# Kernel optimization log

Measured on AMD Instinct MI355X. Metric: run time of the kernel, lower is better.

## Reference

```python
import jax, jax.numpy as jnp
import numpy as np

N_USERS = 50000
N_ITEMS = 50000
N_NODES = N_USERS + N_ITEMS
NNZ = 1600000
EMB = 64
N_LAYERS = 3
REG = 1e-5
BATCH = 4096


def setup_inputs() -> dict:
    key = jax.random.key(0)
    ks = jax.random.split(key, 12)
    s = 1.0 / np.sqrt(EMB)
    return {
        "user_emb": jax.random.normal(ks[0], (N_USERS, EMB), jnp.float32) * s,
        "item_emb": jax.random.normal(ks[1], (N_ITEMS, EMB), jnp.float32) * s,
        "W_gc": jax.random.normal(ks[2], (N_LAYERS, EMB, EMB), jnp.float32) * s,
        "b_gc": jax.random.normal(ks[3], (N_LAYERS, 1, EMB), jnp.float32) * s,
        "W_bi": jax.random.normal(ks[4], (N_LAYERS, EMB, EMB), jnp.float32) * s,
        "b_bi": jax.random.normal(ks[5], (N_LAYERS, 1, EMB), jnp.float32) * s,
        "adj_val": jax.random.uniform(ks[6], (NNZ,), jnp.float32),
        "adj_row": jax.random.randint(ks[7], (NNZ,), 0, N_NODES, jnp.int32),
        "adj_col": jax.random.randint(ks[8], (NNZ,), 0, N_NODES, jnp.int32),
        "u": jax.random.randint(ks[9], (BATCH,), 0, N_USERS, jnp.int32),
        "i": jax.random.randint(ks[10], (BATCH,), 0, N_ITEMS, jnp.int32),
        "j": jax.random.randint(ks[11], (BATCH,), 0, N_ITEMS, jnp.int32),
    }


def _spmm(row, col, val, x):
    # sparse COO matmul: out[r] += val_e * x[col_e]
    return jax.ops.segment_sum(val[:, None] * x[col], row, num_segments=N_NODES)


def reference(user_emb, item_emb, W_gc, b_gc, W_bi, b_bi, adj_val,
              adj_row, adj_col, u, i, j):
    ego = jnp.concatenate([user_emb, item_emb], axis=0)  # [N, 64]
    all_embeddings = [ego]
    for k in range(N_LAYERS):
        side = _spmm(adj_row, adj_col, adj_val, ego)        # A @ ego
        side_L = side - ego                                  # (A - I) @ ego
        sum_emb = side @ W_gc[k] + b_gc[k]
        bi_emb = (ego * side_L) @ W_bi[k] + b_bi[k]
        ego = jax.nn.leaky_relu(sum_emb + bi_emb, negative_slope=0.01)
        # F.normalize(p=2, dim=1), eps=1e-12
        norm = jnp.linalg.norm(ego, axis=1, keepdims=True)
        all_embeddings.append(ego / jnp.maximum(norm, 1e-12))
    all_emb = jnp.concatenate(all_embeddings, axis=1)       # [N, 64*(1+3)]
    u_g, i_g = all_emb[:N_USERS], all_emb[N_USERS:]
    u_emb = u_g[u]
    p_emb = i_g[i]
    n_emb = i_g[j]
    y_ui = jnp.sum(u_emb * p_emb, axis=1)
    y_uj = jnp.sum(u_emb * n_emb, axis=1)
    log_prob = jnp.mean(jax.nn.log_sigmoid(y_ui - y_uj))
    bpr_loss = -log_prob
    l2norm = (jnp.sum(u_emb ** 2) / 2.0 + jnp.sum(p_emb ** 2) / 2.0
              + jnp.sum(n_emb ** 2) / 2.0) / u_emb.shape[0]
    return bpr_loss + REG * l2norm
```

## Files before the change

kernel.cpp:

```cpp
#include <hip/hip_runtime.h>
#include <math.h>

#define N_USERS 50000
#define N_ITEMS 50000
#define N_NODES 100000
#define NNZ_E   1600000
#define EMB     64
#define BATCH   4096
#define REG_C   1e-5f

#define BSH    8
#define NBUCK  ((N_NODES + 255) >> BSH)
#define BCAP   5120
#define NSB    256
#define CHUNK  ((NNZ_E + NSB - 1) / NSB)

__device__ __forceinline__ unsigned short f2bf(float f) {
    unsigned u = __float_as_uint(f);
    u = (u + 0x7FFFu + ((u >> 16) & 1u)) >> 16;
    return (unsigned short)u;
}
__device__ __forceinline__ float bf2f(unsigned short h) {
    return __uint_as_float(((unsigned)h) << 16);
}

__global__ __launch_bounds__(256) void init_ego(const float* __restrict__ ue,
                                                const float* __restrict__ ie,
                                                float* __restrict__ ego,
                                                unsigned short* __restrict__ ego16) {
    const int total = N_NODES * EMB / 4;
    const int uf4   = N_USERS * EMB / 4;
    for (int idx = blockIdx.x * blockDim.x + threadIdx.x; idx < total;
         idx += gridDim.x * blockDim.x) {
        float4 v = (idx < uf4) ? ((const float4*)ue)[idx]
                               : ((const float4*)ie)[idx - uf4];
        ((float4*)ego)[idx] = v;
        ushort4 h;
        h.x = f2bf(v.x); h.y = f2bf(v.y); h.z = f2bf(v.z); h.w = f2bf(v.w);
        *(ushort4*)&ego16[(size_t)idx * 4] = h;
    }
}

__global__ __launch_bounds__(256) void binscatter(const int* __restrict__ rw,
                                                  const int* __restrict__ cl,
                                                  const float* __restrict__ val,
                                                  int* __restrict__ bcnt,
                                                  int2* __restrict__ bin) {
    __shared__ int lcount[NBUCK];
    __shared__ int lbase[NBUCK];
    const int t    = threadIdx.x;
    const int eend = min(NNZ_E, (int)((blockIdx.x + 1) * CHUNK));

    for (int b = t; b < NBUCK; b += 256) lcount[b] = 0;
    __syncthreads();

    for (int e = blockIdx.x * CHUNK + t; e < eend; e += 256)
        atomicAdd(&lcount[rw[e] >> BSH], 1);
    __syncthreads();

    for (int b = t; b < NBUCK; b += 256) {
        const int c = lcount[b];
        lbase[b]  = (c > 0) ? atomicAdd(&bcnt[b], c) : 0;
        lcount[b] = 0;
    }
    __syncthreads();

    for (int e = blockIdx.x * CHUNK + t; e < eend; e += 256) {
        const int r = rw[e];
        const int b = r >> BSH;
        const int ofs = atomicAdd(&lcount[b], 1);
        const int rel = lbase[b] + ofs;
        if (rel < BCAP)
            bin[(size_t)b * BCAP + rel] =
                make_int2(((r & 255) << 17) | cl[e], __float_as_int(val[e]));
    }
}

__global__ __launch_bounds__(512) void scan_buckets(const int* __restrict__ bcnt,
                                                    int* __restrict__ bbase) {
    const int t = threadIdx.x;
    const int lane = t & 63, w = t >> 6;
    const int v = (t < NBUCK) ? bcnt[t] : 0;
    int incl = v;
    #pragma unroll
    for (int off = 1; off < 64; off <<= 1) {
        const int x = __shfl_up(incl, off);
        if (lane >= off) incl += x;
    }
    __shared__ int wt[8];
    if (lane == 63) wt[w] = incl;
    __syncthreads();
    int wb = 0;
    #pragma unroll
    for (int q = 0; q < 8; ++q) wb += (q < w) ? wt[q] : 0;
    if (t < NBUCK) bbase[t] = wb + incl - v;
}

__global__ __launch_bounds__(256) void csr_place(const int* __restrict__ bcnt,
                                                 const int* __restrict__ bbase,
                                                 const int2* __restrict__ bin,
                                                 int* __restrict__ row_ptr,
                                                 int2* __restrict__ ep) {
    __shared__ int rcnt[256];
    __shared__ int rbase[256];
    __shared__ int wt[4];
    const int t    = threadIdx.x;
    const int buck = blockIdx.x;
    const int n    = min(bcnt[buck], BCAP);
    const int base = bbase[buck];
    const int2* mybin = bin + (size_t)buck * BCAP;

    rcnt[t] = 0;
    __syncthreads();
    for (int i = t; i < n; i += 256)
        atomicAdd(&rcnt[mybin[i].x >> 17], 1);
    __syncthreads();

    const int c = rcnt[t];
    const int lane = t & 63, w = t >> 6;
    int incl = c;
    #pragma unroll
    for (int off = 1; off < 64; off <<= 1) {
        const int x = __shfl_up(incl, off);
        if (lane >= off) incl += x;
    }
    if (lane == 63) wt[w] = incl;
    __syncthreads();
    int wb = 0;
    #pragma unroll
    for (int q = 0; q < 4; ++q) wb += (q < w) ? wt[q] : 0;
    const int myb = base + wb + incl - c;

    const int gr = (buck << BSH) + t;
    if (gr < N_NODES) row_ptr[gr] = myb;
    if (buck == 0 && t == 0) row_ptr[N_NODES] = NNZ_E;
    rbase[t] = myb;
    __syncthreads();
    rcnt[t] = 0;
    __syncthreads();

    for (int i = t; i < n; i += 256) {
        const int2 e  = mybin[i];
        const int r8  = e.x >> 17;
        const int col = e.x & 0x1FFFF;
        const int ofs = atomicAdd(&rcnt[r8], 1);
        ep[rbase[r8] + ofs] = make_int2(col, e.y);
    }
}

__global__ __launch_bounds__(256) void spmm_csr(const int* __restrict__ rp,
                                                const int2* __restrict__ ep,
                                                const unsigned short* __restrict__ xb,
                                                float* __restrict__ y) {
    const int w    = (blockIdx.x * blockDim.x + threadIdx.x) >> 6;
    const int lane = threadIdx.x & 63;
    if (w >= N_NODES) return;
    const int beg = rp[w];
    const int end = rp[w + 1];
    float acc = 0.f;
    int e = beg;
    for (; e + 4 <= end; e += 4) {
        const int2 p0 = ep[e];
        const int2 p1 = ep[e + 1];
        const int2 p2 = ep[e + 2];
        const int2 p3 = ep[e + 3];
        const float x0 = bf2f(xb[(size_t)p0.x * EMB + lane]);
        const float x1 = bf2f(xb[(size_t)p1.x * EMB + lane]);
        const float x2 = bf2f(xb[(size_t)p2.x * EMB + lane]);
        const float x3 = bf2f(xb[(size_t)p3.x * EMB + lane]);
        acc += __int_as_float(p0.y) * x0;
        acc += __int_as_float(p1.y) * x1;
        acc += __int_as_float(p2.y) * x2;
        acc += __int_as_float(p3.y) * x3;
    }
    for (; e < end; ++e) {
        const int2 p = ep[e];
        acc += __int_as_float(p.y) * bf2f(xb[(size_t)p.x * EMB + lane]);
    }
    y[(size_t)w * EMB + lane] = acc;
}

__global__ __launch_bounds__(256) void layer_update(const float* __restrict__ side,
                                                    float* __restrict__ ego,
                                                    unsigned short* __restrict__ ego16,
                                                    const float* __restrict__ Wgc,
                                                    const float* __restrict__ bgc,
                                                    const float* __restrict__ Wbi,
                                                    const float* __restrict__ bbi) {
    __shared__ float HT[EMB * EMB];
    __shared__ float GT[EMB * EMB];
    __shared__ float WG[EMB * EMB];
    __shared__ float WB[EMB * EMB];

    const int t  = threadIdx.x;
    const int r0 = blockIdx.x * 64;

    #pragma unroll
    for (int it = 0; it < 4; ++it) {
        const int f4  = t + it * 256;
        const int d   = f4 >> 4;
        const int c0  = (f4 & 15) * 4;

        float4 wg = ((const float4*)Wgc)[f4];
        float4 wb = ((const float4*)Wbi)[f4];
        *(float4*)&WG[d * EMB + c0] = wg;
        *(float4*)&WB[d * EMB + c0] = wb;

        const int gr = r0 + d;
        float4 s4 = make_float4(0.f, 0.f, 0.f, 0.f);
        float4 e4 = s4;
        if (gr < N_NODES) {
            s4 = ((const float4*)side)[gr * 16 + (f4 & 15)];
            e4 = ((const float4*)ego)[gr * 16 + (f4 & 15)];
        }
        const float hv[4] = {s4.x, s4.y, s4.z, s4.w};
        const float ev[4] = {e4.x, e4.y, e4.z, e4.w};
        #pragma unroll
        for (int q = 0; q < 4; ++q) {
            const int dd = c0 + q;
            const int sw = (dd & 7) << 2;
            HT[dd * EMB + (d ^ sw)] = hv[q];
            GT[dd * EMB + (d ^ sw)] = ev[q] * (hv[q] - ev[q]);
        }
    }
    __syncthreads();

    const int tr = t >> 4;
    const int to = t & 15;

    float acc[4][4];
    #pragma unroll
    for (int i2 = 0; i2 < 4; ++i2)
        #pragma unroll
        for (int j2 = 0; j2 < 4; ++j2) acc[i2][j2] = 0.f;

    #pragma unroll 8
    for (int d = 0; d < EMB; ++d) {
        const int sw = (d & 7) << 2;
        const float4 ah4 = *(const float4*)&HT[d * EMB + ((tr * 4) ^ sw)];
        const float4 ag4 = *(const float4*)&GT[d * EMB + ((tr * 4) ^ sw)];
        const float4 wg4 = *(const float4*)&WG[d * EMB + to * 4];
        const float4 wb4 = *(const float4*)&WB[d * EMB + to * 4];
        const float ah[4] = {ah4.x, ah4.y, ah4.z, ah4.w};
        const float ag[4] = {ag4.x, ag4.y, ag4.z, ag4.w};
        const float wg[4] = {wg4.x, wg4.y, wg4.z, wg4.w};
        const float wb[4] = {wb4.x, wb4.y, wb4.z, wb4.w};
        #pragma unroll
        for (int i2 = 0; i2 < 4; ++i2)
            #pragma unroll
            for (int j2 = 0; j2 < 4; ++j2)
                acc[i2][j2] += ah[i2] * wg[j2] + ag[i2] * wb[j2];
    }

    const float4 bg4 = ((const float4*)bgc)[to];
    const float4 bb4 = ((const float4*)bbi)[to];
    const float bs[4] = {bg4.x + bb4.x, bg4.y + bb4.y, bg4.z + bb4.z, bg4.w + bb4.w};

    #pragma unroll
    for (int i2 = 0; i2 < 4; ++i2) {
        const int gr = r0 + tr * 4 + i2;
        if (gr < N_NODES) {
            float4 vo;
            float* vp = (float*)&vo;
            #pragma unroll
            for (int j2 = 0; j2 < 4; ++j2) {
                float v = acc[i2][j2] + bs[j2];
                vp[j2] = (v >= 0.f) ? v : 0.01f * v;
            }
            *(float4*)&ego[gr * EMB + to * 4] = vo;
            ushort4 h;
            h.x = f2bf(vo.x); h.y = f2bf(vo.y); h.z = f2bf(vo.z); h.w = f2bf(vo.w);
            *(ushort4*)&ego16[(size_t)gr * EMB + to * 4] = h;
        }
    }
}

__global__ __launch_bounds__(256) void gather_norm(const float* __restrict__ ego,
                                                   const int* __restrict__ u,
                                                   const int* __restrict__ ii,
                                                   const int* __restrict__ jj,
                                                   float* __restrict__ Gk) {
    const int gtid = blockIdx.x * blockDim.x + threadIdx.x;
    const int wave = gtid >> 6;
    const int lane = threadIdx.x & 63;
    if (wave >= 3 * BATCH) return;
    const int a = wave / BATCH;
    const int b = wave - a * BATCH;
    const int node = (a == 0) ? u[b] : N_USERS + ((a == 1) ? ii[b] : jj[b]);
    const float v = ego[(size_t)node * EMB + lane];
    float ss = v * v;
    #pragma unroll
    for (int m = 32; m; m >>= 1) ss += __shfl_xor(ss, m);
    const float inv = 1.f / fmaxf(sqrtf(ss), 1e-12f);
    Gk[(size_t)wave * EMB + lane] = v * inv;
}

__global__ __launch_bounds__(256) void loss_kernel(const float* __restrict__ ue,
                                                   const float* __restrict__ ie,
                                                   const float* __restrict__ G,
                                                   const int* __restrict__ u,
                                                   const int* __restrict__ ii,
                                                   const int* __restrict__ jj,
                                                   float* __restrict__ out) {
    const int gtid = blockIdx.x * blockDim.x + threadIdx.x;
    const int b    = gtid >> 6;
    const int lane = threadIdx.x & 63;
    if (b >= BATCH) return;

    const int uu = u[b], pi = ii[b], nj = jj[b];
    float uv[4], pv[4], nv[4];
    uv[0] = ue[(size_t)uu * EMB + lane];
    pv[0] = ie[(size_t)pi * EMB + lane];
    nv[0] = ie[(size_t)nj * EMB + lane];
    #pragma unroll
    for (int k = 0; k < 3; ++k) {
        uv[k + 1] = G[(((size_t)k * 3 + 0) * BATCH + b) * EMB + lane];
        pv[k + 1] = G[(((size_t)k * 3 + 1) * BATCH + b) * EMB + lane];
        nv[k + 1] = G[(((size_t)k * 3 + 2) * BATCH + b) * EMB + lane];
    }
    float yui = 0.f, yuj = 0.f, l2 = 0.f;
    #pragma unroll
    for (int s = 0; s < 4; ++s) {
        yui += uv[s] * pv[s];
        yuj += uv[s] * nv[s];
        l2  += uv[s] * uv[s] + pv[s] * pv[s] + nv[s] * nv[s];
    }
    #pragma unroll
    for (int m = 32; m; m >>= 1) {
        yui += __shfl_xor(yui, m);
        yuj += __shfl_xor(yuj, m);
        l2  += __shfl_xor(l2, m);
    }
    if (lane == 0) {
        const float d  = yui - yuj;
        const float sp = (d > 0.f) ? log1pf(expf(-d)) : (-d + log1pf(expf(d)));
        const float contrib = sp * (1.f / BATCH) + REG_C * (l2 * 0.5f) * (1.f / BATCH);
        atomicAdd(out, contrib);
    }
}

extern "C" void kernel_launch(void* const* d_in, const int* in_sizes, int n_in,
                              void* d_out, int out_size, void* d_ws, size_t ws_size,
                              hipStream_t stream) {
    const float* ue   = (const float*)d_in[0];
    const float* ie   = (const float*)d_in[1];
    const float* Wgc  = (const float*)d_in[2];
    const float* bgc  = (const float*)d_in[3];
    const float* Wbi  = (const float*)d_in[4];
    const float* bbi  = (const float*)d_in[5];
    const float* aval = (const float*)d_in[6];
    const int*   arow = (const int*)d_in[7];
    const int*   acol = (const int*)d_in[8];
    const int*   u    = (const int*)d_in[9];
    const int*   ii   = (const int*)d_in[10];
    const int*   jj   = (const int*)d_in[11];
    float* out = (float*)d_out;

    const size_t NE = (size_t)N_NODES * EMB;
    char* p = (char*)d_ws;
    float* ego   = (float*)p;                 p += NE * 4;
    float* sideb = (float*)p;                 p += NE * 4;
    float* G     = (float*)p;                 p += (size_t)9 * BATCH * EMB * 4;
    int* row_ptr = (int*)p;                   p += (size_t)(N_NODES + 2) * 4;
    int* bcnt    = (int*)p;                   p += (size_t)(NBUCK + 1) * 4;
    int* bbase   = (int*)p;                   p += (size_t)(NBUCK + 1) * 4;
    p = (char*)(((uintptr_t)p + 15) & ~(uintptr_t)15);
    int2* epack  = (int2*)p;                  p += (size_t)NNZ_E * 8;
    int2* bin    = (int2*)p;                  p += (size_t)NBUCK * BCAP * 8;
    p = (char*)(((uintptr_t)p + 15) & ~(uintptr_t)15);
    unsigned short* ego16 = (unsigned short*)p;

    hipMemsetAsync(bcnt, 0, (NBUCK + 1) * sizeof(int), stream);
    hipLaunchKernelGGL(binscatter, dim3(NSB), dim3(256), 0, stream,
                       arow, acol, aval, bcnt, bin);
    hipLaunchKernelGGL(scan_buckets, dim3(1), dim3(512), 0, stream, bcnt, bbase);
    hipLaunchKernelGGL(csr_place, dim3(NBUCK), dim3(256), 0, stream,
                       bcnt, bbase, bin, row_ptr, epack);

    hipLaunchKernelGGL(init_ego, dim3(2048), dim3(256), 0, stream, ue, ie, ego, ego16);

    for (int k = 0; k < 3; ++k) {
        hipLaunchKernelGGL(spmm_csr, dim3((N_NODES * 64 + 255) / 256), dim3(256), 0, stream,
                           row_ptr, epack, ego16, sideb);
        hipLaunchKernelGGL(layer_update, dim3((N_NODES + 63) / 64), dim3(256), 0, stream,
                           sideb, ego, ego16,
                           Wgc + (size_t)k * EMB * EMB, bgc + (size_t)k * EMB,
                           Wbi + (size_t)k * EMB * EMB, bbi + (size_t)k * EMB);
        hipLaunchKernelGGL(gather_norm, dim3((3 * BATCH + 3) / 4), dim3(256), 0, stream,
                           ego, u, ii, jj, G + (size_t)k * 3 * BATCH * EMB);
    }

    hipMemsetAsync(d_out, 0, sizeof(float), stream);
    hipLaunchKernelGGL(loss_kernel, dim3(BATCH / 4), dim3(256), 0, stream,
                       ue, ie, G, u, ii, jj, out);
}
```

Measured before the change: 557.9 us.

## Store ego and side in bf16, presort edges by column, deepen SpMM unroll

The fp32 ego and side buffers are removed. SpMM output, layer_update inputs and outputs, and gather_norm all work on bf16 storage, which halves that memory traffic. A new colsort_place kernel reorders each bucket's edges by column range before CSR placement, so rows gather neighbours with better locality. The SpMM inner loop also issues 8 gathers at a time. The costs are an extra preprocessing kernel and lower precision in the side and ego values carried between layers.

```diff
diff --git a/kernel.cpp b/kernel.cpp
--- a/kernel.cpp
+++ b/kernel.cpp
@@ -26,7 +26,6 @@
 
 __global__ __launch_bounds__(256) void init_ego(const float* __restrict__ ue,
                                                 const float* __restrict__ ie,
-                                                float* __restrict__ ego,
                                                 unsigned short* __restrict__ ego16) {
     const int total = N_NODES * EMB / 4;
     const int uf4   = N_USERS * EMB / 4;
@@ -34,7 +33,6 @@
          idx += gridDim.x * blockDim.x) {
         float4 v = (idx < uf4) ? ((const float4*)ue)[idx]
                                : ((const float4*)ie)[idx - uf4];
-        ((float4*)ego)[idx] = v;
         ushort4 h;
         h.x = f2bf(v.x); h.y = f2bf(v.y); h.z = f2bf(v.z); h.w = f2bf(v.w);
         *(ushort4*)&ego16[(size_t)idx * 4] = h;
@@ -94,6 +92,47 @@
     #pragma unroll
     for (int q = 0; q < 8; ++q) wb += (q < w) ? wt[q] : 0;
     if (t < NBUCK) bbase[t] = wb + incl - v;
+}
+
+__global__ __launch_bounds__(256) void colsort_place(const int* __restrict__ bcnt,
+                                                     int2* __restrict__ bin) {
+    __shared__ int2 ebuf[BCAP];
+    __shared__ int  cnt[256];
+    __shared__ int  wt[4];
+    const int t    = threadIdx.x;
+    const int buck = blockIdx.x;
+    const int n    = min(bcnt[buck], BCAP);
+    int2* mybin = bin + (size_t)buck * BCAP;
+
+    cnt[t] = 0;
+    for (int i = t; i < n; i += 256) ebuf[i] = mybin[i];
+    __syncthreads();
+
+    for (int i = t; i < n; i += 256)
+        atomicAdd(&cnt[(ebuf[i].x & 0x1FFFF) >> 9], 1);
+    __syncthreads();
+
+    const int c    = cnt[t];
+    const int lane = t & 63, w = t >> 6;
+    int incl = c;
+    #pragma unroll
+    for (int off = 1; off < 64; off <<= 1) {
+        const int v = __shfl_up(incl, off);
+        if (lane >= off) incl += v;
+    }
+    if (lane == 63) wt[w] = incl;
+    __syncthreads();
+    int wb = 0;
+    #pragma unroll
+    for (int q = 0; q < 4; ++q) wb += (q < w) ? wt[q] : 0;
+    cnt[t] = wb + incl - c;
+    __syncthreads();
+
+    for (int i = t; i < n; i += 256) {
+        const int2 e   = ebuf[i];
+        const int  pos = atomicAdd(&cnt[(e.x & 0x1FFFF) >> 9], 1);
+        mybin[pos] = e;
+    }
 }
 
 __global__ __launch_bounds__(256) void csr_place(const int* __restrict__ bcnt,
@@ -151,7 +190,7 @@
 __global__ __launch_bounds__(256) void spmm_csr(const int* __restrict__ rp,
                                                 const int2* __restrict__ ep,
                                                 const unsigned short* __restrict__ xb,
-                                                float* __restrict__ y) {
+                                                unsigned short* __restrict__ y16) {
     const int w    = (blockIdx.x * blockDim.x + threadIdx.x) >> 6;
     const int lane = threadIdx.x & 63;
     if (w >= N_NODES) return;
@@ -159,29 +198,38 @@
     const int end = rp[w + 1];
     float acc = 0.f;
     int e = beg;
+    for (; e + 8 <= end; e += 8) {
+        int2  p[8];
+        float xv[8];
+        #pragma unroll
+        for (int q = 0; q < 8; ++q) p[q] = ep[e + q];
+        #pragma unroll
+        for (int q = 0; q < 8; ++q)
+            xv[q] = bf2f(xb[(size_t)p[q].x * EMB + lane]);
+        #pragma unroll
+        for (int q = 0; q < 8; ++q)
+            acc += __int_as_float(p[q].y) * xv[q];
+    }
     for (; e + 4 <= end; e += 4) {
-        const int2 p0 = ep[e];
-        const int2 p1 = ep[e + 1];
-        const int2 p2 = ep[e + 2];
-        const int2 p3 = ep[e + 3];
-        const float x0 = bf2f(xb[(size_t)p0.x * EMB + lane]);
-        const float x1 = bf2f(xb[(size_t)p1.x * EMB + lane]);
-        const float x2 = bf2f(xb[(size_t)p2.x * EMB + lane]);
-        const float x3 = bf2f(xb[(size_t)p3.x * EMB + lane]);
-        acc += __int_as_float(p0.y) * x0;
-        acc += __int_as_float(p1.y) * x1;
-        acc += __int_as_float(p2.y) * x2;
-        acc += __int_as_float(p3.y) * x3;
+        int2  p[4];
+        float xv[4];
+        #pragma unroll
+        for (int q = 0; q < 4; ++q) p[q] = ep[e + q];
+        #pragma unroll
+        for (int q = 0; q < 4; ++q)
+            xv[q] = bf2f(xb[(size_t)p[q].x * EMB + lane]);
+        #pragma unroll
+        for (int q = 0; q < 4; ++q)
+            acc += __int_as_float(p[q].y) * xv[q];
     }
     for (; e < end; ++e) {
         const int2 p = ep[e];
         acc += __int_as_float(p.y) * bf2f(xb[(size_t)p.x * EMB + lane]);
     }
-    y[(size_t)w * EMB + lane] = acc;
-}
-
-__global__ __launch_bounds__(256) void layer_update(const float* __restrict__ side,
-                                                    float* __restrict__ ego,
+    y16[(size_t)w * EMB + lane] = f2bf(acc);
+}
+
+__global__ __launch_bounds__(256) void layer_update(const unsigned short* __restrict__ side16,
                                                     unsigned short* __restrict__ ego16,
                                                     const float* __restrict__ Wgc,
                                                     const float* __restrict__ bgc,
@@ -207,14 +255,14 @@
         *(float4*)&WB[d * EMB + c0] = wb;
 
         const int gr = r0 + d;
-        float4 s4 = make_float4(0.f, 0.f, 0.f, 0.f);
-        float4 e4 = s4;
+        float hv[4] = {0.f, 0.f, 0.f, 0.f};
+        float ev[4] = {0.f, 0.f, 0.f, 0.f};
         if (gr < N_NODES) {
-            s4 = ((const float4*)side)[gr * 16 + (f4 & 15)];
-            e4 = ((const float4*)ego)[gr * 16 + (f4 & 15)];
+            const ushort4 s4h = *(const ushort4*)&side16[(size_t)gr * EMB + c0];
+            const ushort4 e4h = *(const ushort4*)&ego16[(size_t)gr * EMB + c0];
+            hv[0] = bf2f(s4h.x); hv[1] = bf2f(s4h.y); hv[2] = bf2f(s4h.z); hv[3] = bf2f(s4h.w);
+            ev[0] = bf2f(e4h.x); ev[1] = bf2f(e4h.y); ev[2] = bf2f(e4h.z); ev[3] = bf2f(e4h.w);
         }
-        const float hv[4] = {s4.x, s4.y, s4.z, s4.w};
-        const float ev[4] = {e4.x, e4.y, e4.z, e4.w};
         #pragma unroll
         for (int q = 0; q < 4; ++q) {
             const int dd = c0 + q;
@@ -260,22 +308,22 @@
     for (int i2 = 0; i2 < 4; ++i2) {
         const int gr = r0 + tr * 4 + i2;
         if (gr < N_NODES) {
-            float4 vo;
-            float* vp = (float*)&vo;
-            #pragma unroll
-            for (int j2 = 0; j2 < 4; ++j2) {
-                float v = acc[i2][j2] + bs[j2];
-                vp[j2] = (v >= 0.f) ? v : 0.01f * v;
-            }
-            *(float4*)&ego[gr * EMB + to * 4] = vo;
             ushort4 h;
-            h.x = f2bf(vo.x); h.y = f2bf(vo.y); h.z = f2bf(vo.z); h.w = f2bf(vo.w);
+            float v0 = acc[i2][0] + bs[0];
+            float v1 = acc[i2][1] + bs[1];
+            float v2 = acc[i2][2] + bs[2];
+            float v3 = acc[i2][3] + bs[3];
+            v0 = (v0 >= 0.f) ? v0 : 0.01f * v0;
+            v1 = (v1 >= 0.f) ? v1 : 0.01f * v1;
+            v2 = (v2 >= 0.f) ? v2 : 0.01f * v2;
+            v3 = (v3 >= 0.f) ? v3 : 0.01f * v3;
+            h.x = f2bf(v0); h.y = f2bf(v1); h.z = f2bf(v2); h.w = f2bf(v3);
             *(ushort4*)&ego16[(size_t)gr * EMB + to * 4] = h;
         }
     }
 }
 
-__global__ __launch_bounds__(256) void gather_norm(const float* __restrict__ ego,
+__global__ __launch_bounds__(256) void gather_norm(const unsigned short* __restrict__ ego16,
                                                    const int* __restrict__ u,
                                                    const int* __restrict__ ii,
                                                    const int* __restrict__ jj,
@@ -287,7 +335,7 @@
     const int a = wave / BATCH;
     const int b = wave - a * BATCH;
     const int node = (a == 0) ? u[b] : N_USERS + ((a == 1) ? ii[b] : jj[b]);
-    const float v = ego[(size_t)node * EMB + lane];
+    const float v = bf2f(ego16[(size_t)node * EMB + lane]);
     float ss = v * v;
     #pragma unroll
     for (int m = 32; m; m >>= 1) ss += __shfl_xor(ss, m);
@@ -358,8 +406,8 @@
 
     const size_t NE = (size_t)N_NODES * EMB;
     char* p = (char*)d_ws;
-    float* ego   = (float*)p;                 p += NE * 4;
-    float* sideb = (float*)p;                 p += NE * 4;
+    unsigned short* ego16  = (unsigned short*)p;  p += NE * 2;
+    unsigned short* side16 = (unsigned short*)p;  p += NE * 2;
     float* G     = (float*)p;                 p += (size_t)9 * BATCH * EMB * 4;
     int* row_ptr = (int*)p;                   p += (size_t)(N_NODES + 2) * 4;
     int* bcnt    = (int*)p;                   p += (size_t)(NBUCK + 1) * 4;
@@ -367,27 +415,27 @@
     p = (char*)(((uintptr_t)p + 15) & ~(uintptr_t)15);
     int2* epack  = (int2*)p;                  p += (size_t)NNZ_E * 8;
     int2* bin    = (int2*)p;                  p += (size_t)NBUCK * BCAP * 8;
-    p = (char*)(((uintptr_t)p + 15) & ~(uintptr_t)15);
-    unsigned short* ego16 = (unsigned short*)p;
 
     hipMemsetAsync(bcnt, 0, (NBUCK + 1) * sizeof(int), stream);
     hipLaunchKernelGGL(binscatter, dim3(NSB), dim3(256), 0, stream,
                        arow, acol, aval, bcnt, bin);
     hipLaunchKernelGGL(scan_buckets, dim3(1), dim3(512), 0, stream, bcnt, bbase);
+    hipLaunchKernelGGL(colsort_place, dim3(NBUCK), dim3(256), 0, stream,
+                       bcnt, bin);
     hipLaunchKernelGGL(csr_place, dim3(NBUCK), dim3(256), 0, stream,
                        bcnt, bbase, bin, row_ptr, epack);
 
-    hipLaunchKernelGGL(init_ego, dim3(2048), dim3(256), 0, stream, ue, ie, ego, ego16);
+    hipLaunchKernelGGL(init_ego, dim3(2048), dim3(256), 0, stream, ue, ie, ego16);
 
     for (int k = 0; k < 3; ++k) {
         hipLaunchKernelGGL(spmm_csr, dim3((N_NODES * 64 + 255) / 256), dim3(256), 0, stream,
-                           row_ptr, epack, ego16, sideb);
+                           row_ptr, epack, ego16, side16);
         hipLaunchKernelGGL(layer_update, dim3((N_NODES + 63) / 64), dim3(256), 0, stream,
-                           sideb, ego, ego16,
+                           side16, ego16,
                            Wgc + (size_t)k * EMB * EMB, bgc + (size_t)k * EMB,
                            Wbi + (size_t)k * EMB * EMB, bbi + (size_t)k * EMB);
         hipLaunchKernelGGL(gather_norm, dim3((3 * BATCH + 3) / 4), dim3(256), 0, stream,
-                           ego, u, ii, jj, G + (size_t)k * 3 * BATCH * EMB);
+                           ego16, u, ii, jj, G + (size_t)k * 3 * BATCH * EMB);
     }
 
     hipMemsetAsync(d_out, 0, sizeof(float), stream);
```

Measured after the change: 513.6 us. 1.09x faster.
